# Kernel optimization log

Hardware: AMD Instinct MI355X
Metric: run time of the kernel (lower is better)

Reference implementation:

```python
import jax, jax.numpy as jnp
import numpy as np

B, S, T, H, E = 64, 256, 128, 1024, 512


def setup_inputs() -> dict:
    key = jax.random.key(0)
    ks = jax.random.split(key, 16)
    sc = 0.02
    inp = {
        "trg_embed": jax.random.normal(ks[0], (B, T, E), jnp.float32),
        "encoder_hidden": jax.random.normal(ks[1], (B, S, 2 * H), jnp.float32),
        "encoder_final": jax.random.normal(ks[2], (1, B, 2 * H), jnp.float32),
        "src_mask": jnp.ones((B, 1, S), dtype=bool),
        "trg_mask": jnp.ones((B, 1, T), dtype=bool),
        # bridge: Linear(2H -> H, bias)
        "W_bridge": jax.random.normal(ks[3], (H, 2 * H), jnp.float32) * sc,
        "b_bridge": jnp.zeros((H,), jnp.float32),
        # Bahdanau attention: key/query/energy layers (no bias)
        "W_key": jax.random.normal(ks[4], (H, 2 * H), jnp.float32) * sc,
        "W_query": jax.random.normal(ks[5], (H, H), jnp.float32) * sc,
        "v_energy": jax.random.normal(ks[6], (H,), jnp.float32) * sc,
        # GRU (1 layer): input size E + 2H, hidden H. PyTorch gate order [r, z, n].
        "W_ih": jax.random.normal(ks[7], (3 * H, E + 2 * H), jnp.float32) * sc,
        "W_hh": jax.random.normal(ks[8], (3 * H, H), jnp.float32) * sc,
        "b_ih": jnp.zeros((3 * H,), jnp.float32),
        "b_hh": jnp.zeros((3 * H,), jnp.float32),
        # pre_output: Linear(H + 2H + E -> H, no bias)
        "W_pre": jax.random.normal(ks[9], (H, H + 2 * H + E), jnp.float32) * sc,
    }
    return inp


def reference(trg_embed, encoder_hidden, encoder_final, src_mask, trg_mask,
              W_bridge, b_bridge, W_key, W_query, v_energy,
              W_ih, W_hh, b_ih, b_hh, W_pre):
    neg_inf = jnp.float32(-1e9)
    # init_hidden: tanh(bridge(encoder_final)) -> [num_layers, B, H]; take last layer
    h0 = jnp.tanh(jnp.einsum('lbk,hk->lbh', encoder_final, W_bridge) + b_bridge)[-1]  # [B, H]
    # precompute projected keys once (as in forward())
    proj_key = jnp.einsum('bsk,hk->bsh', encoder_hidden, W_key)  # [B, S, H]
    mask = src_mask[:, 0, :]  # [B, S]

    def step(h, prev_embed):  # h: [B,H], prev_embed: [B,E]
        # Bahdanau attention with query = last-layer hidden state
        q = h @ W_query.T                                        # [B, H]
        energies = jnp.tanh(q[:, None, :] + proj_key) @ v_energy  # [B, S]
        energies = jnp.where(mask, energies, neg_inf)
        alphas = jax.nn.softmax(energies, axis=-1)               # [B, S]
        context = jnp.einsum('bs,bsd->bd', alphas, encoder_hidden)  # [B, 2H]
        # GRU step on concat(prev_embed, context)
        x = jnp.concatenate([prev_embed, context], axis=-1)      # [B, E+2H]
        gi = x @ W_ih.T + b_ih                                   # [B, 3H]
        gh = h @ W_hh.T + b_hh                                   # [B, 3H]
        i_r, i_z, i_n = jnp.split(gi, 3, axis=-1)
        h_r, h_z, h_n = jnp.split(gh, 3, axis=-1)
        r = jax.nn.sigmoid(i_r + h_r)
        z = jax.nn.sigmoid(i_z + h_z)
        n = jnp.tanh(i_n + r * h_n)
        h_new = (1.0 - z) * n + z * h                            # [B, H]
        # pre-output projection (dropout disabled: eval / p effectively identity)
        pre = jnp.concatenate([prev_embed, h_new, context], axis=-1) @ W_pre.T  # [B, H]
        return h_new, (h_new, pre)

    h_final, (states, pres) = jax.lax.scan(step, h0, jnp.swapaxes(trg_embed, 0, 1))
    decoder_states = jnp.swapaxes(states, 0, 1)      # [B, T, H]
    pre_output_vectors = jnp.swapaxes(pres, 0, 1)    # [B, T, H]
    hidden = h_final[None]                            # [num_layers=1, B, H]
    return decoder_states, hidden, pre_output_vectors
```

## Files before the change

### kernel.cpp

```cpp
#include <hip/hip_runtime.h>

#define Bn 64
#define Sn 256
#define Tn 128
#define Hn 1024
#define En 512
#define H2n 2048
#define NBLK 256
#define NTHR 1024

#define WCTX 10
#define WH 12

#define GW 0
#define PWc 0
#define PWh 32768
#define PWq 49152
#define PWe 65536
#define PREP 73728
#define SCR2 75776
#define SCR 147456
#define GIL 155648
#define LDS_BYTES 161792

typedef __attribute__((ext_vector_type(8))) short short8v;
typedef __attribute__((ext_vector_type(4))) float floatx4;

__device__ __forceinline__ unsigned short f2bf(float f) {
  union { float f; unsigned u; } x; x.f = f;
  unsigned r = x.u + 0x7fffu + ((x.u >> 16) & 1u);
  return (unsigned short)(r >> 16);
}
__device__ __forceinline__ float bf2f(unsigned short u) {
  union { unsigned u; float f; } x; x.u = ((unsigned)u) << 16; return x.f;
}
__device__ __forceinline__ float sigm(float x) { return 1.f / (1.f + __expf(-x)); }
__device__ __forceinline__ float tanh_f(float x) {
  float e = __expf(2.f * x);
  return 1.f - 2.f / (e + 1.f);
}
__device__ __forceinline__ short8v ldf(const unsigned short* p) { return *(const short8v*)p; }
#define MFMA(a, b, c) __builtin_amdgcn_mfma_f32_16x16x32_bf16(a, b, c, 0, 0, 0)

__device__ __forceinline__ float ldc_f(const float* p) {
  return __hip_atomic_load(p, __ATOMIC_RELAXED, __HIP_MEMORY_SCOPE_AGENT);
}
__device__ __forceinline__ void stc_f(float* p, float v) {
  __hip_atomic_store(p, v, __ATOMIC_RELAXED, __HIP_MEMORY_SCOPE_AGENT);
}
__device__ __forceinline__ void stc_u32(unsigned* p, unsigned v) {
  __hip_atomic_store(p, v, __ATOMIC_RELAXED, __HIP_MEMORY_SCOPE_AGENT);
}
__device__ __forceinline__ unsigned long long ldc_u64(const unsigned long long* p) {
  return __hip_atomic_load(p, __ATOMIC_RELAXED, __HIP_MEMORY_SCOPE_AGENT);
}
__device__ __forceinline__ void stc_u64(unsigned long long* p, unsigned long long v) {
  __hip_atomic_store(p, v, __ATOMIC_RELAXED, __HIP_MEMORY_SCOPE_AGENT);
}

__device__ __forceinline__ short8v packf(const float* p) {
  float4 e0 = *(const float4*)p, e1 = *(const float4*)(p + 4);
  short8v x;
  x[0] = (short)f2bf(e0.x); x[1] = (short)f2bf(e0.y);
  x[2] = (short)f2bf(e0.z); x[3] = (short)f2bf(e0.w);
  x[4] = (short)f2bf(e1.x); x[5] = (short)f2bf(e1.y);
  x[6] = (short)f2bf(e1.z); x[7] = (short)f2bf(e1.w);
  return x;
}

__global__ __launch_bounds__(256) void cast_kernel(const float4* __restrict__ src,
                                                   uint2* __restrict__ dst, int n4) {
  for (int i = blockIdx.x * blockDim.x + threadIdx.x; i < n4; i += gridDim.x * blockDim.x) {
    float4 v = src[i];
    uint2 p;
    p.x = (unsigned)f2bf(v.x) | ((unsigned)f2bf(v.y) << 16);
    p.y = (unsigned)f2bf(v.z) | ((unsigned)f2bf(v.w) << 16);
    dst[i] = p;
  }
}

__global__ __launch_bounds__(256) void bridge_kernel(const float* __restrict__ ef,
                                                     const float* __restrict__ Wb,
                                                     const float* __restrict__ bb,
                                                     float* __restrict__ h0out,
                                                     unsigned short* __restrict__ hb0) {
  __shared__ float efs[H2n];
  const int b = blockIdx.x >> 2, jq = blockIdx.x & 3;
  const int j = jq * 256 + threadIdx.x;
  for (int i = threadIdx.x; i < H2n; i += 256) efs[i] = ef[(size_t)b * H2n + i];
  __syncthreads();
  const float* wr = Wb + (size_t)j * H2n;
  float acc = bb[j];
  for (int k = 0; k < H2n; k += 4) {
    float4 wv = *(const float4*)&wr[k];
    acc += efs[k] * wv.x + efs[k + 1] * wv.y + efs[k + 2] * wv.z + efs[k + 3] * wv.w;
  }
  float th = tanhf(acc);
  h0out[(size_t)b * Hn + j] = th;
  hb0[(size_t)b * Hn + j] = f2bf(th);
}

__global__ __launch_bounds__(256) void pk_gemm(const unsigned short* __restrict__ A,
                                               const unsigned short* __restrict__ Bw,
                                               unsigned short* __restrict__ pk) {
  const int bid = blockIdx.x;
  const int mt = bid >> 4, nt = bid & 15;
  const int w = threadIdx.x >> 6, lane = threadIdx.x & 63;
  const int lm = lane & 15, lk = lane >> 4, ko = lk * 8;
  const unsigned short* arow = A + (size_t)(mt * 64 + w * 16 + lm) * 2048 + ko;
  const unsigned short* b0 = Bw + (size_t)(nt * 64 + lm) * 2048 + ko;
  const unsigned short* b1 = Bw + (size_t)(nt * 64 + 16 + lm) * 2048 + ko;
  const unsigned short* b2 = Bw + (size_t)(nt * 64 + 32 + lm) * 2048 + ko;
  const unsigned short* b3 = Bw + (size_t)(nt * 64 + 48 + lm) * 2048 + ko;
  floatx4 c0 = {0,0,0,0}, c1 = {0,0,0,0}, c2 = {0,0,0,0}, c3 = {0,0,0,0};
  for (int k = 0; k < 2048; k += 32) {
    short8v a = ldf(arow + k);
    c0 = MFMA(a, ldf(b0 + k), c0);
    c1 = MFMA(a, ldf(b1 + k), c1);
    c2 = MFMA(a, ldf(b2 + k), c2);
    c3 = MFMA(a, ldf(b3 + k), c3);
  }
  const int m = mt * 64 + w * 16 + lk * 4;
  const int j = nt * 64 + lm;
#pragma unroll
  for (int r = 0; r < 4; ++r) {
    unsigned short* row = pk + (size_t)(m + r) * 1024 + j;
    row[0]  = f2bf(c0[r]);
    row[16] = f2bf(c1[r]);
    row[32] = f2bf(c2[r]);
    row[48] = f2bf(c3[r]);
  }
}

struct DA {
  const float* emb; const float* v; const float* bih; const float* bhh;
  const unsigned short* pk; const unsigned short* ehb;
  const unsigned short* Wih; const unsigned short* Whh;
  const unsigned short* Wpre; const unsigned short* Wq;
  float* hbuf; unsigned short* hbR; float* qbuf; float* wbuf; float* psump;
  unsigned short* ctxR; unsigned* bar; float* out;
};

__device__ __forceinline__ void gbar(unsigned* bar, int tid, unsigned idx, int inv) {
  asm volatile("s_waitcnt vmcnt(0)" ::: "memory");
  __syncthreads();
  if (tid == 0) {
    unsigned old = __hip_atomic_fetch_add(bar, 1u, __ATOMIC_RELAXED, __HIP_MEMORY_SCOPE_AGENT);
    if (old + 1u == (unsigned)NBLK * idx) {
      __hip_atomic_store(bar + 32, idx, __ATOMIC_RELAXED, __HIP_MEMORY_SCOPE_AGENT);
    } else {
      unsigned g;
      do {
        __builtin_amdgcn_s_sleep(2);
        g = __hip_atomic_load(bar + 32, __ATOMIC_RELAXED, __HIP_MEMORY_SCOPE_AGENT);
      } while (g < idx);
    }
  }
  __syncthreads();
  if (inv) __builtin_amdgcn_fence(__ATOMIC_ACQUIRE, "agent");
}

__device__ __forceinline__ void phA(const DA& a, char* dsm, int bid, int tid,
                                    int w, int lane, int t) {
  const int b = bid >> 2, sc4 = bid & 3;
  float* w_s = (float*)(dsm + SCR);
  float* q_s = (float*)(dsm + SCR + 1024);
  if (tid < 256) {
    const unsigned long long* qp = (const unsigned long long*)(a.qbuf + (size_t)b * Hn) + tid * 2;
    unsigned long long u0 = ldc_u64(qp), u1 = ldc_u64(qp + 1);
    union { unsigned long long u; float f[2]; } x0, x1; x0.u = u0; x1.u = u1;
    q_s[tid * 4] = x0.f[0]; q_s[tid * 4 + 1] = x0.f[1];
    q_s[tid * 4 + 2] = x1.f[0]; q_s[tid * 4 + 3] = x1.f[1];
  }
  __syncthreads();
  float qr[16], vr[16];
  const float* vp = a.v + lane * 16;
#pragma unroll
  for (int i = 0; i < 16; i += 4) {
    *(float4*)&qr[i] = *(const float4*)&q_s[lane * 16 + i];
    *(float4*)&vr[i] = *(const float4*)(vp + i);
  }
  short8v p0[4], p1[4];
#pragma unroll
  for (int i = 0; i < 4; ++i) {
    const unsigned short* prow = a.pk + ((size_t)b * Sn + sc4 * 64 + w * 4 + i) * Hn + lane * 16;
    p0[i] = ldf(prow); p1[i] = ldf(prow + 8);
  }
#pragma unroll
  for (int i = 0; i < 4; ++i) {
    float ep = 0.f;
#pragma unroll
    for (int e = 0; e < 8; ++e) {
      ep += vr[e] * tanh_f(qr[e] + bf2f((unsigned short)p0[i][e]));
      ep += vr[8 + e] * tanh_f(qr[8 + e] + bf2f((unsigned short)p1[i][e]));
    }
#pragma unroll
    for (int m = 1; m < 64; m <<= 1) ep += __shfl_xor(ep, m, 64);
    if (lane == 0) {
      float wv = __expf(ep - 20.f);
      w_s[w * 4 + i] = wv;
      stc_f(a.wbuf + (size_t)b * Sn + sc4 * 64 + w * 4 + i, wv);
    }
  }
  __syncthreads();
  if (tid < 64) {
    float wv = w_s[tid];
#pragma unroll
    for (int m = 1; m < 64; m <<= 1) wv += __shfl_xor(wv, m, 64);
    if (tid == 0) stc_f(a.psump + sc4 * 64 + b, wv);
  }
  asm volatile("s_waitcnt vmcnt(0)" ::: "memory");
  __syncthreads();
  if (tid == 0) stc_u32(&a.bar[64 + (b << 2) + sc4], (unsigned)(t + 1));
  if (tid < 4) {
    while (__hip_atomic_load(&a.bar[64 + (b << 2) + tid], __ATOMIC_RELAXED,
                             __HIP_MEMORY_SCOPE_AGENT) < (unsigned)(t + 1))
      __builtin_amdgcn_s_sleep(1);
  }
  __syncthreads();
  const int dq = sc4;
  float* wn = (float*)(dsm + SCR);
  float psinv = 1.f / (ldc_f(a.psump + b) + ldc_f(a.psump + 64 + b) +
                       ldc_f(a.psump + 128 + b) + ldc_f(a.psump + 192 + b));
  if (tid < 256) wn[tid] = ldc_f(a.wbuf + (size_t)b * Sn + tid) * psinv;
  __syncthreads();
  const int ls = lane >> 2, ldcx = lane & 3;
  const int dchunk = w * 4 + ldcx;
  const unsigned short* ebase = a.ehb + (size_t)b * Sn * H2n + dq * 512 + dchunk * 8;
  float acc[8] = {};
#pragma unroll
  for (int k = 0; k < 16; ++k) {
    const int s = ls + k * 16;
    short8v e = ldf(ebase + (size_t)s * H2n);
    float wf = wn[s];
#pragma unroll
    for (int e2 = 0; e2 < 8; ++e2) acc[e2] += wf * bf2f((unsigned short)e[e2]);
  }
#pragma unroll
  for (int m = 4; m < 64; m <<= 1) {
#pragma unroll
    for (int e2 = 0; e2 < 8; ++e2) acc[e2] += __shfl_xor(acc[e2], m, 64);
  }
  if (ls == 0) {
    union { unsigned long long u[2]; unsigned short s[8]; } p;
#pragma unroll
    for (int e2 = 0; e2 < 8; ++e2) p.s[e2] = f2bf(acc[e2]);
    unsigned long long* dst = (unsigned long long*)(
        a.ctxR + (size_t)(t % WCTX) * Bn * H2n + (size_t)b * H2n + dq * 512 + dchunk * 8);
    stc_u64(dst, p.u[0]); stc_u64(dst + 1, p.u[1]);
  }
}

__device__ __forceinline__ void gate_c(const DA& a, char* dsm, int j0, int w,
                                       int lane, int tid, int t, int cur, int nxt) {
  float* scr = (float*)(dsm + SCR);
  for (int i = tid; i < 2048; i += NTHR) scr[i] = 0.f;
  __syncthreads();
  const int mt = w & 3, ks = w >> 2;
  const int lm = lane & 15, lk = lane >> 4;
  const int arow = mt * 16 + lm, jb = lm & 7;
  const unsigned short* ctxrow =
      a.ctxR + (size_t)(t % WCTX) * Bn * H2n + (size_t)arow * H2n + lk * 8;
  const unsigned short* hrow =
      a.hbR + (size_t)(t % WH) * Bn * Hn + (size_t)arow * Hn + lk * 8;
  const char* wb0 = dsm + GW + (size_t)((0 * 8 + jb) * 384) * 16;
  const char* wb1 = dsm + GW + (size_t)((1 * 8 + jb) * 384) * 16;
  const char* wb2 = dsm + GW + (size_t)((2 * 8 + jb) * 384) * 16;
  floatx4 ar = {0,0,0,0}, az = {0,0,0,0}, ain = {0,0,0,0}, ahn = {0,0,0,0};
#pragma unroll 4
  for (int kc = ks * 24; kc < ks * 24 + 24; ++kc) {
    short8v x = (kc < 64) ? ldf(ctxrow + kc * 32) : ldf(hrow + (kc - 64) * 32);
    const size_t slot = (size_t)((kc * 4 + lk) ^ jb) * 16;
    ar = MFMA(x, *(const short8v*)(wb0 + slot), ar);
    az = MFMA(x, *(const short8v*)(wb1 + slot), az);
    if (kc < 64) ain = MFMA(x, *(const short8v*)(wb2 + slot), ain);
    else         ahn = MFMA(x, *(const short8v*)(wb2 + slot), ahn);
  }
  if (lm < 8) {
#pragma unroll
    for (int r = 0; r < 4; ++r) {
      const int bb = mt * 16 + lk * 4 + r;
      atomicAdd(&scr[(0 * 64 + bb) * 8 + jb], ar[r]);
      atomicAdd(&scr[(1 * 64 + bb) * 8 + jb], az[r]);
      atomicAdd(&scr[(2 * 64 + bb) * 8 + jb], ain[r]);
      atomicAdd(&scr[(3 * 64 + bb) * 8 + jb], ahn[r]);
    }
  }
  __syncthreads();
  if (tid < 256) {
    const int bb = tid >> 2, jj = (tid & 3) * 2;
    float* gil = (float*)(dsm + GIL);
    float hn2[2];
#pragma unroll
    for (int u = 0; u < 2; ++u) {
      const int j = jj + u, jg = j0 + j;
      float grv = scr[(0 * 64 + bb) * 8 + j] + gil[(0 * 64 + bb) * 8 + j] + a.bhh[jg];
      float gzv = scr[(1 * 64 + bb) * 8 + j] + gil[(1 * 64 + bb) * 8 + j] + a.bhh[Hn + jg];
      float ginv = scr[(2 * 64 + bb) * 8 + j] + gil[(2 * 64 + bb) * 8 + j];
      float ghnv = scr[(3 * 64 + bb) * 8 + j] + a.bhh[2 * Hn + jg];
      float rr = sigm(grv), zz = sigm(gzv);
      float nn = tanh_f(ginv + rr * ghnv);
      float hold = a.hbuf[(size_t)cur * Bn * Hn + (size_t)bb * Hn + jg];
      float hnew = (1.f - zz) * nn + zz * hold;
      hn2[u] = hnew;
      a.hbuf[(size_t)nxt * Bn * Hn + (size_t)bb * Hn + jg] = hnew;
      a.out[((size_t)bb * Tn + t) * Hn + jg] = hnew;
      if (t == Tn - 1) a.out[(size_t)Bn * Tn * Hn + (size_t)bb * Hn + jg] = hnew;
    }
    unsigned hpack = (unsigned)f2bf(hn2[0]) | ((unsigned)f2bf(hn2[1]) << 16);
    stc_u32((unsigned*)(a.hbR + (size_t)((t + 1) % WH) * Bn * Hn +
                        (size_t)bb * Hn + j0 + jj), hpack);
  }
}

__device__ __forceinline__ void pre_c(const DA& a, char* dsm, int j0, int w,
                                      int lane, int tid, int t) {
  float* prep = (float*)(dsm + PREP);
  for (int i = tid; i < 512; i += NTHR) prep[i] = 0.f;
  __syncthreads();
  const int mt = w & 3, ks = w >> 2;
  const int lm = lane & 15, lk = lane >> 4;
  const int arow = mt * 16 + lm, jb = lm & 7;
  const unsigned short* ctxrow =
      a.ctxR + (size_t)(t % WCTX) * Bn * H2n + (size_t)arow * H2n + lk * 8;
  const float* ep = a.emb + ((size_t)arow * Tn + t) * En + lk * 8;
  const char* we = dsm + PWe + (size_t)(jb * 64) * 16;
  const char* wc = dsm + PWc + (size_t)(jb * 256) * 16;
  floatx4 acc = {0,0,0,0};
#pragma unroll 4
  for (int kc = ks * 20; kc < ks * 20 + 20; ++kc) {
    if (kc < 16) {
      acc = MFMA(packf(ep + kc * 32),
                 *(const short8v*)(we + (size_t)((kc * 4 + lk) ^ jb) * 16), acc);
    } else {
      const int c = kc - 16;
      acc = MFMA(ldf(ctxrow + c * 32),
                 *(const short8v*)(wc + (size_t)((c * 4 + lk) ^ jb) * 16), acc);
    }
  }
  if (lm < 8) {
#pragma unroll
    for (int r = 0; r < 4; ++r)
      atomicAdd(&prep[(mt * 16 + lk * 4 + r) * 8 + jb], acc[r]);
  }
  __syncthreads();
}

__device__ __forceinline__ void pre_d(const DA& a, char* dsm, int j0, int w,
                                      int lane, int tid, int t, int hslot, int doPre) {
  float* scr = (float*)(dsm + SCR2);
  for (int i = tid; i < 1024; i += NTHR) scr[i] = 0.f;
  __syncthreads();
  const int mt = w & 3, part = w >> 2;
  const int lm = lane & 15, lk = lane >> 4;
  const int arow = mt * 16 + lm, jb = lm & 7;
  const unsigned short* hrow =
      a.hbR + (size_t)hslot * Bn * Hn + (size_t)arow * Hn + lk * 8;
  const int isQ = part >> 1;
  const char* wbase = dsm + (isQ ? PWq : PWh) + (size_t)(jb * 128) * 16;
  if (doPre || isQ) {
    floatx4 acc = {0,0,0,0};
    const int k0 = (part & 1) * 16;
#pragma unroll 4
    for (int kh = k0; kh < k0 + 16; ++kh)
      acc = MFMA(ldf(hrow + kh * 32),
                 *(const short8v*)(wbase + (size_t)((kh * 4 + lk) ^ jb) * 16), acc);
    if (lm < 8) {
#pragma unroll
      for (int r = 0; r < 4; ++r)
        atomicAdd(&scr[(isQ * 64 + mt * 16 + lk * 4 + r) * 8 + jb], acc[r]);
    }
  }
  __syncthreads();
  if (tid < 256) {
    const int bb = tid >> 2, jj = (tid & 3) * 2;
    float* prep = (float*)(dsm + PREP);
#pragma unroll
    for (int u = 0; u < 2; ++u) {
      const int j = jj + u, jg = j0 + j;
      if (doPre) {
        float pv = scr[(0 * 64 + bb) * 8 + j] + prep[bb * 8 + j];
        a.out[(size_t)Bn * Tn * Hn + (size_t)Bn * Hn + ((size_t)bb * Tn + t) * Hn + jg] = pv;
      }
      stc_f(a.qbuf + (size_t)bb * Hn + jg, scr[(1 * 64 + bb) * 8 + j]);
    }
  }
}

__device__ __forceinline__ void gi_compute(const DA& a, char* dsm, int j0, int w,
                                           int lane, int t1) {
  const int mt = w & 3, g = w >> 2;
  if (g >= 3) return;
  const int lm = lane & 15, lk = lane >> 4;
  const int arow = mt * 16 + lm;
  const unsigned short* wrow = a.Wih + (size_t)(g * Hn + j0 + (lm & 7)) * 2560 + lk * 8;
  const float* ep = a.emb + ((size_t)arow * Tn + t1) * En + lk * 8;
  floatx4 acc = {0,0,0,0};
#pragma unroll 4
  for (int kk = 0; kk < 16; ++kk)
    acc = MFMA(packf(ep + kk * 32), ldf(wrow + kk * 32), acc);
  if (lm < 8) {
    float* gil = (float*)(dsm + GIL);
    float bv = a.bih[g * Hn + j0 + lm];
#pragma unroll
    for (int r = 0; r < 4; ++r)
      gil[(g * 64 + mt * 16 + lk * 4 + r) * 8 + lm] = acc[r] + bv;
  }
}

__global__ void __launch_bounds__(NTHR, 4) dec_kernel(DA a) {
  extern __shared__ char dsm[];
  const int tid = threadIdx.x, bid = blockIdx.x;
  const int w = tid >> 6, lane = tid & 63;
  const bool isGate = bid < 128;
  const int j0 = (isGate ? bid : bid - 128) * 8;

  if (isGate) {
    for (int idx = tid; idx < 9216; idx += NTHR) {
      int row = idx / 384, c = idx % 384;
      int g = row >> 3, j = row & 7;
      const unsigned short* src = (c < 256)
          ? a.Wih + (size_t)(g * Hn + j0 + j) * 2560 + 512 + c * 8
          : a.Whh + (size_t)(g * Hn + j0 + j) * Hn + (c - 256) * 8;
      *(uint4*)(dsm + (size_t)(row * 384 + (c ^ j)) * 16) = *(const uint4*)src;
    }
  } else {
    for (int idx = tid; idx < 4608; idx += NTHR) {
      const unsigned short* src; size_t dst;
      if (idx < 2048) {
        int j = idx >> 8, c = idx & 255;
        src = a.Wpre + (size_t)(j0 + j) * 3584 + 1536 + c * 8;
        dst = PWc + (size_t)(j * 256 + (c ^ j)) * 16;
      } else if (idx < 3072) {
        int i = idx - 2048, j = i >> 7, c = i & 127;
        src = a.Wpre + (size_t)(j0 + j) * 3584 + 512 + c * 8;
        dst = PWh + (size_t)(j * 128 + (c ^ j)) * 16;
      } else if (idx < 4096) {
        int i = idx - 3072, j = i >> 7, c = i & 127;
        src = a.Wq + (size_t)(j0 + j) * Hn + c * 8;
        dst = PWq + (size_t)(j * 128 + (c ^ j)) * 16;
      } else {
        int i = idx - 4096, j = i >> 6, c = i & 63;
        src = a.Wpre + (size_t)(j0 + j) * 3584 + c * 8;
        dst = PWe + (size_t)(j * 64 + (c ^ j)) * 16;
      }
      *(uint4*)(dsm + dst) = *(const uint4*)src;
    }
  }
  __syncthreads();

  unsigned bi = 1;
  if (isGate) gi_compute(a, dsm, j0, w, lane, 0);
  else pre_d(a, dsm, j0, w, lane, tid, 0, 0, 0);
  gbar(a.bar, tid, bi++, 0);

  for (int t = 0; t < Tn; ++t) {
    const int cur = t & 1, nxt = cur ^ 1;
    phA(a, dsm, bid, tid, w, lane, t);
    gbar(a.bar, tid, bi++, 0);
    if (isGate) gate_c(a, dsm, j0, w, lane, tid, t, cur, nxt);
    else pre_c(a, dsm, j0, w, lane, tid, t);
    gbar(a.bar, tid, bi++, 0);
    if (isGate) { if (t + 1 < Tn) gi_compute(a, dsm, j0, w, lane, t + 1); }
    else pre_d(a, dsm, j0, w, lane, tid, t, (t + 1) % WH, 1);
    gbar(a.bar, tid, bi++, (t & 7) == 7);
  }
}

extern "C" void kernel_launch(void* const* d_in, const int* in_sizes, int n_in,
                              void* d_out, int out_size, void* d_ws, size_t ws_size,
                              hipStream_t stream) {
  (void)in_sizes; (void)n_in; (void)out_size; (void)ws_size;
  const float* emb = (const float*)d_in[0];
  const float* eh  = (const float*)d_in[1];
  const float* ef  = (const float*)d_in[2];
  const float* Wb  = (const float*)d_in[5];
  const float* bb  = (const float*)d_in[6];
  const float* Wk  = (const float*)d_in[7];
  const float* Wq  = (const float*)d_in[8];
  const float* v   = (const float*)d_in[9];
  const float* Wih = (const float*)d_in[10];
  const float* Whh = (const float*)d_in[11];
  const float* bih = (const float*)d_in[12];
  const float* bhh = (const float*)d_in[13];
  const float* Wpre= (const float*)d_in[14];
  float* out = (float*)d_out;

  char* wsb = (char*)d_ws;
  unsigned short* ehb  = (unsigned short*)(wsb + 0);
  unsigned short* pkb  = (unsigned short*)(wsb + 67108864);
  unsigned short* Wihb = (unsigned short*)(wsb + 100663296);
  unsigned short* Whhb = (unsigned short*)(wsb + 116391936);
  unsigned short* Wpreb= (unsigned short*)(wsb + 122683392);
  unsigned short* Wqb  = (unsigned short*)(wsb + 130023424);
  unsigned short* Wkb  = (unsigned short*)(wsb + 132120576);
  unsigned short* ctxR = (unsigned short*)(wsb + 132120576);
  unsigned short* hbR  = (unsigned short*)(wsb + 134742016);
  float* hbuf = (float*)(wsb + 136314880);
  float* qbuf = (float*)(wsb + 137101312);
  float* wbuf = (float*)(wsb + 137363456);
  float* psump= (float*)(wsb + 137428992);
  unsigned* bar = (unsigned*)(wsb + 137695232);

  hipMemsetAsync(bar, 0, 4096, stream);
  cast_kernel<<<2048, 256, 0, stream>>>((const float4*)eh, (uint2*)ehb, Bn * Sn * H2n / 4);
  cast_kernel<<<2048, 256, 0, stream>>>((const float4*)Wih, (uint2*)Wihb, 3 * Hn * 2560 / 4);
  cast_kernel<<<1024, 256, 0, stream>>>((const float4*)Whh, (uint2*)Whhb, 3 * Hn * Hn / 4);
  cast_kernel<<<1024, 256, 0, stream>>>((const float4*)Wpre, (uint2*)Wpreb, Hn * 3584 / 4);
  cast_kernel<<<512, 256, 0, stream>>>((const float4*)Wq, (uint2*)Wqb, Hn * Hn / 4);
  cast_kernel<<<512, 256, 0, stream>>>((const float4*)Wk, (uint2*)Wkb, Hn * H2n / 4);
  pk_gemm<<<4096, 256, 0, stream>>>(ehb, Wkb, pkb);
  bridge_kernel<<<256, 256, 0, stream>>>(ef, Wb, bb, hbuf, hbR);

  DA da;
  da.emb = emb; da.v = v; da.bih = bih; da.bhh = bhh;
  da.pk = pkb; da.ehb = ehb;
  da.Wih = Wihb; da.Whh = Whhb; da.Wpre = Wpreb; da.Wq = Wqb;
  da.hbuf = hbuf; da.hbR = hbR; da.qbuf = qbuf; da.wbuf = wbuf; da.psump = psump;
  da.ctxR = ctxR; da.bar = bar; da.out = out;

  hipFuncSetAttribute(reinterpret_cast<const void*>(&dec_kernel),
                      hipFuncAttributeMaxDynamicSharedMemorySize, LDS_BYTES);
  void* kp[] = { (void*)&da };
  hipLaunchCooperativeKernel(reinterpret_cast<const void*>(&dec_kernel),
                             dim3(NBLK), dim3(NTHR), kp, LDS_BYTES, stream);
}
```

Measured before the change: 11.80 ms.

## Add 512-block decoder variant streaming weights from global memory with hierarchical barrier

Adds a second persistent cooperative decoder kernel that uses 512 blocks of 512 threads. Each block handles half the batch for an 8-column slice and reads GRU and projection weights straight from global or L2 instead of staging them in LDS, which shrinks shared memory so two blocks fit per CU. It also replaces the single-counter grid barrier with a two-level tree barrier to reduce atomic contention, and splits the attention phase across 8 blocks per batch row. The original 256-block kernel is kept as a fallback when the occupancy query or the launch fails. The trade-off is more global weight traffic per step and more blocks taking part in each barrier.

```diff
diff --git a/kernel.cpp b/kernel.cpp
--- a/kernel.cpp
+++ b/kernel.cpp
@@ -6,22 +6,25 @@
 #define Hn 1024
 #define En 512
 #define H2n 2048
-#define NBLK 256
-#define NTHR 1024
 
 #define WCTX 10
 #define WH 12
 
-#define GW 0
-#define PWc 0
-#define PWh 32768
-#define PWq 49152
-#define PWe 65536
-#define PREP 73728
-#define SCR2 75776
-#define SCR 147456
-#define GIL 155648
-#define LDS_BYTES 161792
+#define K2_GW 0
+#define K2_PWc 0
+#define K2_PWh 32768
+#define K2_PWq 49152
+#define K2_PWe 65536
+#define K2_PREP 73728
+#define K2_SCR2 75776
+#define K2_SCR 147456
+#define K2_GIL 155648
+#define K2_LDS 161792
+#define K5_SCR 0
+#define K5_SCR2 4096
+#define K5_PREP 6144
+#define K5_GIL 7168
+#define K5_LDS 10240
 
 typedef __attribute__((ext_vector_type(8))) short short8v;
 typedef __attribute__((ext_vector_type(4))) float floatx4;
@@ -141,12 +144,315 @@
   unsigned short* ctxR; unsigned* bar; float* out;
 };
 
-__device__ __forceinline__ void gbar(unsigned* bar, int tid, unsigned idx, int inv) {
+
+__device__ __forceinline__ void gbar5(unsigned* bar, int tid, int bid, unsigned idx, int inv) {
+  asm volatile("s_waitcnt vmcnt(0)" ::: "memory");
+  __syncthreads();
+  if (tid == 0) {
+    unsigned* leaf = bar + 64 + (bid & 7) * 32;
+    unsigned old = __hip_atomic_fetch_add(leaf, 1u, __ATOMIC_RELAXED, __HIP_MEMORY_SCOPE_AGENT);
+    if (old + 1u == 64u * idx) {
+      unsigned ro = __hip_atomic_fetch_add(bar, 1u, __ATOMIC_RELAXED, __HIP_MEMORY_SCOPE_AGENT);
+      if (ro + 1u == 8u * idx)
+        __hip_atomic_store(bar + 32, idx, __ATOMIC_RELAXED, __HIP_MEMORY_SCOPE_AGENT);
+    }
+    unsigned g;
+    do {
+      g = __hip_atomic_load(bar + 32, __ATOMIC_RELAXED, __HIP_MEMORY_SCOPE_AGENT);
+      if (g >= idx) break;
+      __builtin_amdgcn_s_sleep(2);
+    } while (1);
+  }
+  __syncthreads();
+  if (inv) __builtin_amdgcn_fence(__ATOMIC_ACQUIRE, "agent");
+}
+
+__device__ __forceinline__ void phA5(const DA& a, char* dsm, int bid, int tid,
+                                     int w, int lane, int t) {
+  const int b = bid >> 3, sc8 = bid & 7;
+  float* w_s = (float*)(dsm + K5_SCR);
+  float qr[16], vr[16];
+  {
+    const unsigned long long* qp =
+        (const unsigned long long*)(a.qbuf + (size_t)b * Hn + lane * 16);
+#pragma unroll
+    for (int i = 0; i < 8; ++i) {
+      union { unsigned long long u; float f[2]; } x; x.u = ldc_u64(qp + i);
+      qr[i * 2] = x.f[0]; qr[i * 2 + 1] = x.f[1];
+    }
+    const float* vp = a.v + lane * 16;
+#pragma unroll
+    for (int i = 0; i < 16; i += 4) *(float4*)&vr[i] = *(const float4*)(vp + i);
+  }
+#pragma unroll
+  for (int i = 0; i < 4; ++i) {
+    const unsigned short* prow =
+        a.pk + ((size_t)b * Sn + sc8 * 32 + w * 4 + i) * Hn + lane * 16;
+    short8v p0 = ldf(prow), p1 = ldf(prow + 8);
+    float ep = 0.f;
+#pragma unroll
+    for (int e = 0; e < 8; ++e) {
+      ep += vr[e] * tanh_f(qr[e] + bf2f((unsigned short)p0[e]));
+      ep += vr[8 + e] * tanh_f(qr[8 + e] + bf2f((unsigned short)p1[e]));
+    }
+#pragma unroll
+    for (int m = 1; m < 64; m <<= 1) ep += __shfl_xor(ep, m, 64);
+    if (lane == 0) {
+      float wv = __expf(ep - 20.f);
+      w_s[w * 4 + i] = wv;
+      stc_f(a.wbuf + (size_t)b * Sn + sc8 * 32 + w * 4 + i, wv);
+    }
+  }
+  __syncthreads();
+  if (tid < 32) {
+    float wv = w_s[tid];
+#pragma unroll
+    for (int m = 1; m < 32; m <<= 1) wv += __shfl_xor(wv, m, 64);
+    if (tid == 0) stc_f(a.psump + sc8 * 64 + b, wv);
+  }
+  asm volatile("s_waitcnt vmcnt(0)" ::: "memory");
+  __syncthreads();
+  if (tid == 0) stc_u32(&a.bar[320 + (b << 3) + sc8], (unsigned)(t + 1));
+  if (tid < 8) {
+    while (__hip_atomic_load(&a.bar[320 + (b << 3) + tid], __ATOMIC_RELAXED,
+                             __HIP_MEMORY_SCOPE_AGENT) < (unsigned)(t + 1))
+      __builtin_amdgcn_s_sleep(1);
+  }
+  __syncthreads();
+  float* wn = (float*)(dsm + K5_SCR);
+  float ps = 0.f;
+#pragma unroll
+  for (int k = 0; k < 8; ++k) ps += ldc_f(a.psump + k * 64 + b);
+  float psinv = 1.f / ps;
+  if (tid < 256) wn[tid] = ldc_f(a.wbuf + (size_t)b * Sn + tid) * psinv;
+  __syncthreads();
+  const int ls = lane >> 2, ldcx = lane & 3;
+  const int dchunk = w * 4 + ldcx;
+  const unsigned short* ebase = a.ehb + (size_t)b * Sn * H2n + sc8 * 256 + dchunk * 8;
+  float acc[8] = {};
+#pragma unroll
+  for (int k = 0; k < 16; ++k) {
+    const int s = ls + k * 16;
+    short8v e = ldf(ebase + (size_t)s * H2n);
+    float wf = wn[s];
+#pragma unroll
+    for (int e2 = 0; e2 < 8; ++e2) acc[e2] += wf * bf2f((unsigned short)e[e2]);
+  }
+#pragma unroll
+  for (int m = 4; m < 64; m <<= 1) {
+#pragma unroll
+    for (int e2 = 0; e2 < 8; ++e2) acc[e2] += __shfl_xor(acc[e2], m, 64);
+  }
+  if (ls == 0) {
+    union { unsigned long long u[2]; unsigned short s[8]; } p;
+#pragma unroll
+    for (int e2 = 0; e2 < 8; ++e2) p.s[e2] = f2bf(acc[e2]);
+    unsigned long long* dst = (unsigned long long*)(
+        a.ctxR + (size_t)(t % WCTX) * Bn * H2n + (size_t)b * H2n + sc8 * 256 + dchunk * 8);
+    stc_u64(dst, p.u[0]); stc_u64(dst + 1, p.u[1]);
+  }
+}
+
+__device__ __forceinline__ void gate_c5(const DA& a, char* dsm, int j0, int bh, int w,
+                                        int lane, int tid, int t, int cur, int nxt) {
+  float* scr = (float*)(dsm + K5_SCR);
+  for (int i = tid; i < 1024; i += 512) scr[i] = 0.f;
+  __syncthreads();
+  const int mt = w & 1, ks = w >> 1;
+  const int lm = lane & 15, lk = lane >> 4;
+  const int arow = bh * 32 + mt * 16 + lm, jb = lm & 7;
+  const unsigned short* ctxrow =
+      a.ctxR + (size_t)(t % WCTX) * Bn * H2n + (size_t)arow * H2n + lk * 8;
+  const unsigned short* hrow =
+      a.hbR + (size_t)(t % WH) * Bn * Hn + (size_t)arow * Hn + lk * 8;
+  const unsigned short* bi0 = a.Wih + (size_t)(0 * Hn + j0 + jb) * 2560 + 512 + lk * 8;
+  const unsigned short* bi1 = a.Wih + (size_t)(1 * Hn + j0 + jb) * 2560 + 512 + lk * 8;
+  const unsigned short* bi2 = a.Wih + (size_t)(2 * Hn + j0 + jb) * 2560 + 512 + lk * 8;
+  const unsigned short* bh0 = a.Whh + (size_t)(0 * Hn + j0 + jb) * Hn + lk * 8;
+  const unsigned short* bh1 = a.Whh + (size_t)(1 * Hn + j0 + jb) * Hn + lk * 8;
+  const unsigned short* bh2 = a.Whh + (size_t)(2 * Hn + j0 + jb) * Hn + lk * 8;
+  floatx4 ar = {0,0,0,0}, az = {0,0,0,0}, ain = {0,0,0,0}, ahn = {0,0,0,0};
+#pragma unroll 4
+  for (int kc = ks * 24; kc < ks * 24 + 24; ++kc) {
+    if (kc < 64) {
+      short8v x = ldf(ctxrow + kc * 32);
+      ar  = MFMA(x, ldf(bi0 + kc * 32), ar);
+      az  = MFMA(x, ldf(bi1 + kc * 32), az);
+      ain = MFMA(x, ldf(bi2 + kc * 32), ain);
+    } else {
+      const int c = kc - 64;
+      short8v x = ldf(hrow + c * 32);
+      ar  = MFMA(x, ldf(bh0 + c * 32), ar);
+      az  = MFMA(x, ldf(bh1 + c * 32), az);
+      ahn = MFMA(x, ldf(bh2 + c * 32), ahn);
+    }
+  }
+  if (lm < 8) {
+#pragma unroll
+    for (int r = 0; r < 4; ++r) {
+      const int bb = mt * 16 + lk * 4 + r;
+      atomicAdd(&scr[(0 * 32 + bb) * 8 + jb], ar[r]);
+      atomicAdd(&scr[(1 * 32 + bb) * 8 + jb], az[r]);
+      atomicAdd(&scr[(2 * 32 + bb) * 8 + jb], ain[r]);
+      atomicAdd(&scr[(3 * 32 + bb) * 8 + jb], ahn[r]);
+    }
+  }
+  __syncthreads();
+  if (tid < 128) {
+    const int bb = tid >> 2, jj = (tid & 3) * 2;
+    const int batch = bh * 32 + bb;
+    float* gil = (float*)(dsm + K5_GIL);
+    float hn2[2];
+#pragma unroll
+    for (int u = 0; u < 2; ++u) {
+      const int j = jj + u, jg = j0 + j;
+      float grv = scr[(0 * 32 + bb) * 8 + j] + gil[(0 * 32 + bb) * 8 + j] + a.bhh[jg];
+      float gzv = scr[(1 * 32 + bb) * 8 + j] + gil[(1 * 32 + bb) * 8 + j] + a.bhh[Hn + jg];
+      float ginv = scr[(2 * 32 + bb) * 8 + j] + gil[(2 * 32 + bb) * 8 + j];
+      float ghnv = scr[(3 * 32 + bb) * 8 + j] + a.bhh[2 * Hn + jg];
+      float rr = sigm(grv), zz = sigm(gzv);
+      float nn = tanh_f(ginv + rr * ghnv);
+      float hold = a.hbuf[(size_t)cur * Bn * Hn + (size_t)batch * Hn + jg];
+      float hnew = (1.f - zz) * nn + zz * hold;
+      hn2[u] = hnew;
+      a.hbuf[(size_t)nxt * Bn * Hn + (size_t)batch * Hn + jg] = hnew;
+      a.out[((size_t)batch * Tn + t) * Hn + jg] = hnew;
+      if (t == Tn - 1) a.out[(size_t)Bn * Tn * Hn + (size_t)batch * Hn + jg] = hnew;
+    }
+    unsigned hpack = (unsigned)f2bf(hn2[0]) | ((unsigned)f2bf(hn2[1]) << 16);
+    stc_u32((unsigned*)(a.hbR + (size_t)((t + 1) % WH) * Bn * Hn +
+                        (size_t)batch * Hn + j0 + jj), hpack);
+  }
+}
+
+__device__ __forceinline__ void pre_c5(const DA& a, char* dsm, int j0, int bh, int w,
+                                       int lane, int tid, int t) {
+  float* prep = (float*)(dsm + K5_PREP);
+  for (int i = tid; i < 256; i += 512) prep[i] = 0.f;
+  __syncthreads();
+  const int mt = w & 1, ks = w >> 1;
+  const int lm = lane & 15, lk = lane >> 4;
+  const int arow = bh * 32 + mt * 16 + lm, jb = lm & 7;
+  const unsigned short* ctxrow =
+      a.ctxR + (size_t)(t % WCTX) * Bn * H2n + (size_t)arow * H2n + lk * 8;
+  const float* ep = a.emb + ((size_t)arow * Tn + t) * En + lk * 8;
+  const unsigned short* we = a.Wpre + (size_t)(j0 + jb) * 3584 + lk * 8;
+  const unsigned short* wc = a.Wpre + (size_t)(j0 + jb) * 3584 + 1536 + lk * 8;
+  floatx4 acc = {0,0,0,0};
+#pragma unroll 4
+  for (int kc = ks * 20; kc < ks * 20 + 20; ++kc) {
+    if (kc < 16) {
+      acc = MFMA(packf(ep + kc * 32), ldf(we + kc * 32), acc);
+    } else {
+      const int c = kc - 16;
+      acc = MFMA(ldf(ctxrow + c * 32), ldf(wc + c * 32), acc);
+    }
+  }
+  if (lm < 8) {
+#pragma unroll
+    for (int r = 0; r < 4; ++r)
+      atomicAdd(&prep[(mt * 16 + lk * 4 + r) * 8 + jb], acc[r]);
+  }
+  __syncthreads();
+}
+
+__device__ __forceinline__ void pre_d5(const DA& a, char* dsm, int j0, int bh, int w,
+                                       int lane, int tid, int t, int hslot, int doPre) {
+  float* scr = (float*)(dsm + K5_SCR2);
+  for (int i = tid; i < 512; i += 512) scr[i] = 0.f;
+  __syncthreads();
+  const int mt = w & 1, part = w >> 1;
+  const int lm = lane & 15, lk = lane >> 4;
+  const int arow = bh * 32 + mt * 16 + lm, jb = lm & 7;
+  const unsigned short* hrow =
+      a.hbR + (size_t)hslot * Bn * Hn + (size_t)arow * Hn + lk * 8;
+  const int isQ = part >> 1;
+  const unsigned short* wbase = isQ
+      ? a.Wq + (size_t)(j0 + jb) * Hn + lk * 8
+      : a.Wpre + (size_t)(j0 + jb) * 3584 + 512 + lk * 8;
+  if (doPre || isQ) {
+    floatx4 acc = {0,0,0,0};
+    const int k0 = (part & 1) * 16;
+#pragma unroll 4
+    for (int kh = k0; kh < k0 + 16; ++kh)
+      acc = MFMA(ldf(hrow + kh * 32), ldf(wbase + kh * 32), acc);
+    if (lm < 8) {
+#pragma unroll
+      for (int r = 0; r < 4; ++r)
+        atomicAdd(&scr[(isQ * 32 + mt * 16 + lk * 4 + r) * 8 + jb], acc[r]);
+    }
+  }
+  __syncthreads();
+  if (tid < 128) {
+    const int bb = tid >> 2, jj = (tid & 3) * 2;
+    const int batch = bh * 32 + bb;
+    float* prep = (float*)(dsm + K5_PREP);
+#pragma unroll
+    for (int u = 0; u < 2; ++u) {
+      const int j = jj + u, jg = j0 + j;
+      if (doPre) {
+        float pv = scr[(0 * 32 + bb) * 8 + j] + prep[bb * 8 + j];
+        a.out[(size_t)Bn * Tn * Hn + (size_t)Bn * Hn + ((size_t)batch * Tn + t) * Hn + jg] = pv;
+      }
+      stc_f(a.qbuf + (size_t)batch * Hn + jg, scr[(1 * 32 + bb) * 8 + j]);
+    }
+  }
+}
+
+__device__ __forceinline__ void gi5(const DA& a, char* dsm, int j0, int bh, int w,
+                                    int lane, int t1) {
+  const int mt = w & 1, g = w >> 1;
+  if (g >= 3) return;
+  const int lm = lane & 15, lk = lane >> 4;
+  const int arow = bh * 32 + mt * 16 + lm;
+  const unsigned short* wrow = a.Wih + (size_t)(g * Hn + j0 + (lm & 7)) * 2560 + lk * 8;
+  const float* ep = a.emb + ((size_t)arow * Tn + t1) * En + lk * 8;
+  floatx4 acc = {0,0,0,0};
+#pragma unroll 4
+  for (int kk = 0; kk < 16; ++kk)
+    acc = MFMA(packf(ep + kk * 32), ldf(wrow + kk * 32), acc);
+  if (lm < 8) {
+    float* gil = (float*)(dsm + K5_GIL);
+    float bv = a.bih[g * Hn + j0 + lm];
+#pragma unroll
+    for (int r = 0; r < 4; ++r)
+      gil[(g * 32 + mt * 16 + lk * 4 + r) * 8 + lm] = acc[r] + bv;
+  }
+}
+
+__global__ void __launch_bounds__(512, 4) dec_kernel512(DA a) {
+  extern __shared__ char dsm[];
+  const int tid = threadIdx.x, bid = blockIdx.x;
+  const int w = tid >> 6, lane = tid & 63;
+  const bool isGate = bid < 256;
+  const int rb = isGate ? bid : bid - 256;
+  const int j0 = (rb >> 1) * 8, bh = rb & 1;
+
+  unsigned bi = 1;
+  if (isGate) gi5(a, dsm, j0, bh, w, lane, 0);
+  else pre_d5(a, dsm, j0, bh, w, lane, tid, 0, 0, 0);
+  gbar5(a.bar, tid, bid, bi++, 0);
+
+  for (int t = 0; t < Tn; ++t) {
+    const int cur = t & 1, nxt = cur ^ 1;
+    phA5(a, dsm, bid, tid, w, lane, t);
+    gbar5(a.bar, tid, bid, bi++, 0);
+    if (isGate) gate_c5(a, dsm, j0, bh, w, lane, tid, t, cur, nxt);
+    else pre_c5(a, dsm, j0, bh, w, lane, tid, t);
+    gbar5(a.bar, tid, bid, bi++, 0);
+    if (isGate) { if (t + 1 < Tn) gi5(a, dsm, j0, bh, w, lane, t + 1); }
+    else pre_d5(a, dsm, j0, bh, w, lane, tid, t, (t + 1) % WH, 1);
+    gbar5(a.bar, tid, bid, bi++, (t & 7) == 7);
+  }
+}
+
+
+__device__ __forceinline__ void gbar2(unsigned* bar, int tid, unsigned idx, int inv) {
   asm volatile("s_waitcnt vmcnt(0)" ::: "memory");
   __syncthreads();
   if (tid == 0) {
     unsigned old = __hip_atomic_fetch_add(bar, 1u, __ATOMIC_RELAXED, __HIP_MEMORY_SCOPE_AGENT);
-    if (old + 1u == (unsigned)NBLK * idx) {
+    if (old + 1u == 256u * idx) {
       __hip_atomic_store(bar + 32, idx, __ATOMIC_RELAXED, __HIP_MEMORY_SCOPE_AGENT);
     } else {
       unsigned g;
@@ -160,11 +466,11 @@
   if (inv) __builtin_amdgcn_fence(__ATOMIC_ACQUIRE, "agent");
 }
 
-__device__ __forceinline__ void phA(const DA& a, char* dsm, int bid, int tid,
-                                    int w, int lane, int t) {
+__device__ __forceinline__ void phA2(const DA& a, char* dsm, int bid, int tid,
+                                     int w, int lane, int t) {
   const int b = bid >> 2, sc4 = bid & 3;
-  float* w_s = (float*)(dsm + SCR);
-  float* q_s = (float*)(dsm + SCR + 1024);
+  float* w_s = (float*)(dsm + K2_SCR);
+  float* q_s = (float*)(dsm + K2_SCR + 1024);
   if (tid < 256) {
     const unsigned long long* qp = (const unsigned long long*)(a.qbuf + (size_t)b * Hn) + tid * 2;
     unsigned long long u0 = ldc_u64(qp), u1 = ldc_u64(qp + 1);
@@ -219,7 +525,7 @@
   }
   __syncthreads();
   const int dq = sc4;
-  float* wn = (float*)(dsm + SCR);
+  float* wn = (float*)(dsm + K2_SCR);
   float psinv = 1.f / (ldc_f(a.psump + b) + ldc_f(a.psump + 64 + b) +
                        ldc_f(a.psump + 128 + b) + ldc_f(a.psump + 192 + b));
   if (tid < 256) wn[tid] = ldc_f(a.wbuf + (size_t)b * Sn + tid) * psinv;
@@ -251,10 +557,10 @@
   }
 }
 
-__device__ __forceinline__ void gate_c(const DA& a, char* dsm, int j0, int w,
-                                       int lane, int tid, int t, int cur, int nxt) {
-  float* scr = (float*)(dsm + SCR);
-  for (int i = tid; i < 2048; i += NTHR) scr[i] = 0.f;
+__device__ __forceinline__ void gate_c2(const DA& a, char* dsm, int j0, int w,
+                                        int lane, int tid, int t, int cur, int nxt) {
+  float* scr = (float*)(dsm + K2_SCR);
+  for (int i = tid; i < 2048; i += 1024) scr[i] = 0.f;
   __syncthreads();
   const int mt = w & 3, ks = w >> 2;
   const int lm = lane & 15, lk = lane >> 4;
@@ -263,9 +569,9 @@
       a.ctxR + (size_t)(t % WCTX) * Bn * H2n + (size_t)arow * H2n + lk * 8;
   const unsigned short* hrow =
       a.hbR + (size_t)(t % WH) * Bn * Hn + (size_t)arow * Hn + lk * 8;
-  const char* wb0 = dsm + GW + (size_t)((0 * 8 + jb) * 384) * 16;
-  const char* wb1 = dsm + GW + (size_t)((1 * 8 + jb) * 384) * 16;
-  const char* wb2 = dsm + GW + (size_t)((2 * 8 + jb) * 384) * 16;
+  const char* wb0 = dsm + K2_GW + (size_t)((0 * 8 + jb) * 384) * 16;
+  const char* wb1 = dsm + K2_GW + (size_t)((1 * 8 + jb) * 384) * 16;
+  const char* wb2 = dsm + K2_GW + (size_t)((2 * 8 + jb) * 384) * 16;
   floatx4 ar = {0,0,0,0}, az = {0,0,0,0}, ain = {0,0,0,0}, ahn = {0,0,0,0};
 #pragma unroll 4
   for (int kc = ks * 24; kc < ks * 24 + 24; ++kc) {
@@ -289,7 +595,7 @@
   __syncthreads();
   if (tid < 256) {
     const int bb = tid >> 2, jj = (tid & 3) * 2;
-    float* gil = (float*)(dsm + GIL);
+    float* gil = (float*)(dsm + K2_GIL);
     float hn2[2];
 #pragma unroll
     for (int u = 0; u < 2; ++u) {
@@ -313,10 +619,10 @@
   }
 }
 
-__device__ __forceinline__ void pre_c(const DA& a, char* dsm, int j0, int w,
-                                      int lane, int tid, int t) {
-  float* prep = (float*)(dsm + PREP);
-  for (int i = tid; i < 512; i += NTHR) prep[i] = 0.f;
+__device__ __forceinline__ void pre_c2(const DA& a, char* dsm, int j0, int w,
+                                       int lane, int tid, int t) {
+  float* prep = (float*)(dsm + K2_PREP);
+  for (int i = tid; i < 512; i += 1024) prep[i] = 0.f;
   __syncthreads();
   const int mt = w & 3, ks = w >> 2;
   const int lm = lane & 15, lk = lane >> 4;
@@ -324,8 +630,8 @@
   const unsigned short* ctxrow =
       a.ctxR + (size_t)(t % WCTX) * Bn * H2n + (size_t)arow * H2n + lk * 8;
   const float* ep = a.emb + ((size_t)arow * Tn + t) * En + lk * 8;
-  const char* we = dsm + PWe + (size_t)(jb * 64) * 16;
-  const char* wc = dsm + PWc + (size_t)(jb * 256) * 16;
+  const char* we = dsm + K2_PWe + (size_t)(jb * 64) * 16;
+  const char* wc = dsm + K2_PWc + (size_t)(jb * 256) * 16;
   floatx4 acc = {0,0,0,0};
 #pragma unroll 4
   for (int kc = ks * 20; kc < ks * 20 + 20; ++kc) {
@@ -346,10 +652,10 @@
   __syncthreads();
 }
 
-__device__ __forceinline__ void pre_d(const DA& a, char* dsm, int j0, int w,
-                                      int lane, int tid, int t, int hslot, int doPre) {
-  float* scr = (float*)(dsm + SCR2);
-  for (int i = tid; i < 1024; i += NTHR) scr[i] = 0.f;
+__device__ __forceinline__ void pre_d2(const DA& a, char* dsm, int j0, int w,
+                                       int lane, int tid, int t, int hslot, int doPre) {
+  float* scr = (float*)(dsm + K2_SCR2);
+  for (int i = tid; i < 1024; i += 1024) scr[i] = 0.f;
   __syncthreads();
   const int mt = w & 3, part = w >> 2;
   const int lm = lane & 15, lk = lane >> 4;
@@ -357,7 +663,7 @@
   const unsigned short* hrow =
       a.hbR + (size_t)hslot * Bn * Hn + (size_t)arow * Hn + lk * 8;
   const int isQ = part >> 1;
-  const char* wbase = dsm + (isQ ? PWq : PWh) + (size_t)(jb * 128) * 16;
+  const char* wbase = dsm + (isQ ? K2_PWq : K2_PWh) + (size_t)(jb * 128) * 16;
   if (doPre || isQ) {
     floatx4 acc = {0,0,0,0};
     const int k0 = (part & 1) * 16;
@@ -374,7 +680,7 @@
   __syncthreads();
   if (tid < 256) {
     const int bb = tid >> 2, jj = (tid & 3) * 2;
-    float* prep = (float*)(dsm + PREP);
+    float* prep = (float*)(dsm + K2_PREP);
 #pragma unroll
     for (int u = 0; u < 2; ++u) {
       const int j = jj + u, jg = j0 + j;
@@ -387,8 +693,8 @@
   }
 }
 
-__device__ __forceinline__ void gi_compute(const DA& a, char* dsm, int j0, int w,
-                                           int lane, int t1) {
+__device__ __forceinline__ void gi2(const DA& a, char* dsm, int j0, int w,
+                                    int lane, int t1) {
   const int mt = w & 3, g = w >> 2;
   if (g >= 3) return;
   const int lm = lane & 15, lk = lane >> 4;
@@ -400,7 +706,7 @@
   for (int kk = 0; kk < 16; ++kk)
     acc = MFMA(packf(ep + kk * 32), ldf(wrow + kk * 32), acc);
   if (lm < 8) {
-    float* gil = (float*)(dsm + GIL);
+    float* gil = (float*)(dsm + K2_GIL);
     float bv = a.bih[g * Hn + j0 + lm];
 #pragma unroll
     for (int r = 0; r < 4; ++r)
@@ -408,7 +714,7 @@
   }
 }
 
-__global__ void __launch_bounds__(NTHR, 4) dec_kernel(DA a) {
+__global__ void __launch_bounds__(1024, 4) dec_kernel256(DA a) {
   extern __shared__ char dsm[];
   const int tid = threadIdx.x, bid = blockIdx.x;
   const int w = tid >> 6, lane = tid & 63;
@@ -416,7 +722,7 @@
   const int j0 = (isGate ? bid : bid - 128) * 8;
 
   if (isGate) {
-    for (int idx = tid; idx < 9216; idx += NTHR) {
+    for (int idx = tid; idx < 9216; idx += 1024) {
       int row = idx / 384, c = idx % 384;
       int g = row >> 3, j = row & 7;
       const unsigned short* src = (c < 256)
@@ -425,24 +731,24 @@
       *(uint4*)(dsm + (size_t)(row * 384 + (c ^ j)) * 16) = *(const uint4*)src;
     }
   } else {
-    for (int idx = tid; idx < 4608; idx += NTHR) {
+    for (int idx = tid; idx < 4608; idx += 1024) {
       const unsigned short* src; size_t dst;
       if (idx < 2048) {
         int j = idx >> 8, c = idx & 255;
         src = a.Wpre + (size_t)(j0 + j) * 3584 + 1536 + c * 8;
-        dst = PWc + (size_t)(j * 256 + (c ^ j)) * 16;
+        dst = K2_PWc + (size_t)(j * 256 + (c ^ j)) * 16;
       } else if (idx < 3072) {
         int i = idx - 2048, j = i >> 7, c = i & 127;
         src = a.Wpre + (size_t)(j0 + j) * 3584 + 512 + c * 8;
-        dst = PWh + (size_t)(j * 128 + (c ^ j)) * 16;
+        dst = K2_PWh + (size_t)(j * 128 + (c ^ j)) * 16;
       } else if (idx < 4096) {
         int i = idx - 3072, j = i >> 7, c = i & 127;
         src = a.Wq + (size_t)(j0 + j) * Hn + c * 8;
-        dst = PWq + (size_t)(j * 128 + (c ^ j)) * 16;
+        dst = K2_PWq + (size_t)(j * 128 + (c ^ j)) * 16;
       } else {
         int i = idx - 4096, j = i >> 6, c = i & 63;
         src = a.Wpre + (size_t)(j0 + j) * 3584 + c * 8;
-        dst = PWe + (size_t)(j * 64 + (c ^ j)) * 16;
+        dst = K2_PWe + (size_t)(j * 64 + (c ^ j)) * 16;
       }
       *(uint4*)(dsm + dst) = *(const uint4*)src;
     }
@@ -450,20 +756,20 @@
   __syncthreads();
 
   unsigned bi = 1;
-  if (isGate) gi_compute(a, dsm, j0, w, lane, 0);
-  else pre_d(a, dsm, j0, w, lane, tid, 0, 0, 0);
-  gbar(a.bar, tid, bi++, 0);
+  if (isGate) gi2(a, dsm, j0, w, lane, 0);
+  else pre_d2(a, dsm, j0, w, lane, tid, 0, 0, 0);
+  gbar2(a.bar, tid, bi++, 0);
 
   for (int t = 0; t < Tn; ++t) {
     const int cur = t & 1, nxt = cur ^ 1;
-    phA(a, dsm, bid, tid, w, lane, t);
-    gbar(a.bar, tid, bi++, 0);
-    if (isGate) gate_c(a, dsm, j0, w, lane, tid, t, cur, nxt);
-    else pre_c(a, dsm, j0, w, lane, tid, t);
-    gbar(a.bar, tid, bi++, 0);
-    if (isGate) { if (t + 1 < Tn) gi_compute(a, dsm, j0, w, lane, t + 1); }
-    else pre_d(a, dsm, j0, w, lane, tid, t, (t + 1) % WH, 1);
-    gbar(a.bar, tid, bi++, (t & 7) == 7);
+    phA2(a, dsm, bid, tid, w, lane, t);
+    gbar2(a.bar, tid, bi++, 0);
+    if (isGate) gate_c2(a, dsm, j0, w, lane, tid, t, cur, nxt);
+    else pre_c2(a, dsm, j0, w, lane, tid, t);
+    gbar2(a.bar, tid, bi++, 0);
+    if (isGate) { if (t + 1 < Tn) gi2(a, dsm, j0, w, lane, t + 1); }
+    else pre_d2(a, dsm, j0, w, lane, tid, t, (t + 1) % WH, 1);
+    gbar2(a.bar, tid, bi++, (t & 7) == 7);
   }
 }
 
@@ -519,9 +825,23 @@
   da.hbuf = hbuf; da.hbR = hbR; da.qbuf = qbuf; da.wbuf = wbuf; da.psump = psump;
   da.ctxR = ctxR; da.bar = bar; da.out = out;
 
-  hipFuncSetAttribute(reinterpret_cast<const void*>(&dec_kernel),
-                      hipFuncAttributeMaxDynamicSharedMemorySize, LDS_BYTES);
+  hipFuncSetAttribute(reinterpret_cast<const void*>(&dec_kernel512),
+                      hipFuncAttributeMaxDynamicSharedMemorySize, K5_LDS);
+  hipFuncSetAttribute(reinterpret_cast<const void*>(&dec_kernel256),
+                      hipFuncAttributeMaxDynamicSharedMemorySize, K2_LDS);
+
+  int maxb = 0;
+  hipError_t qe = hipOccupancyMaxActiveBlocksPerMultiprocessor(
+      &maxb, reinterpret_cast<const void*>(&dec_kernel512), 512, (size_t)K5_LDS);
+  bool use512 = (qe == hipSuccess && maxb >= 2);
+  hipError_t le = hipErrorUnknown;
   void* kp[] = { (void*)&da };
-  hipLaunchCooperativeKernel(reinterpret_cast<const void*>(&dec_kernel),
-                             dim3(NBLK), dim3(NTHR), kp, LDS_BYTES, stream);
-}
+  if (use512) {
+    le = hipLaunchCooperativeKernel(reinterpret_cast<const void*>(&dec_kernel512),
+                                    dim3(512), dim3(512), kp, K5_LDS, stream);
+  }
+  if (!use512 || le != hipSuccess) {
+    hipLaunchCooperativeKernel(reinterpret_cast<const void*>(&dec_kernel256),
+                               dim3(256), dim3(1024), kp, K2_LDS, stream);
+  }
+}
```

After: 11.79 ms. Within noise of the previous version (-0.1%).
